# Performance work log

Measured on AMD Instinct MI355X. Metric: run time of the kernel, lower is better.

Reference implementation:

```python
import jax, jax.numpy as jnp
import numpy as np

B, S = 2, 2048
N_DIM, N_HEADS = 2048, 16
Q_RANK, KV_RANK = 1536, 512
ROPE, NOPE, VD = 64, 128, 128
QK_HEAD = NOPE + ROPE  # 192
EPS = 1e-6


def _rmsnorm(x, w, eps=EPS):
    xf = x.astype(jnp.float32)
    norm = xf * jax.lax.rsqrt(jnp.mean(xf * xf, axis=-1, keepdims=True) + eps)
    return norm.astype(x.dtype) * w


def setup_inputs() -> dict:
    key = jax.random.key(0)
    ks = jax.random.split(key, 7)
    std = 0.006
    x = jax.random.normal(ks[0], (B, S, N_DIM), dtype=jnp.float32)
    # rotary frequencies: complex cis encoded as (cos, sin) pairs, [S, ROPE//2, 2]
    inv_freq = 1.0 / (10000.0 ** (np.arange(0, ROPE, 2, dtype=np.float32) / ROPE))
    t = np.arange(S, dtype=np.float32)
    ang = np.outer(t, inv_freq)  # [S, ROPE//2]
    freqs_cis = jnp.asarray(np.stack([np.cos(ang), np.sin(ang)], axis=-1))
    return {
        "x": x,
        "freqs_cis": freqs_cis,
        "wq_a": jax.random.normal(ks[1], (Q_RANK, N_DIM)) * std,
        "q_norm_w": jnp.ones((Q_RANK,), jnp.float32),
        "wq_b": jax.random.normal(ks[2], (N_HEADS * QK_HEAD, Q_RANK)) * std,
        "wkv_a": jax.random.normal(ks[3], (KV_RANK + ROPE, N_DIM)) * std,
        "kv_norm_w": jnp.ones((KV_RANK,), jnp.float32),
        "wkv_b": jax.random.normal(ks[4], (N_HEADS * (NOPE + VD), KV_RANK)) * std,
        "wo": jax.random.normal(ks[5], (N_DIM, N_HEADS * VD)) * std,
    }


def _apply_rope(x_pe, freqs_cis):
    # x_pe: [B, S, H, ROPE] viewed as complex pairs; freqs_cis: [S, ROPE//2, 2]
    xr = x_pe[..., 0::2].astype(jnp.float32)
    xi = x_pe[..., 1::2].astype(jnp.float32)
    cos = freqs_cis[None, :, None, :, 0]
    sin = freqs_cis[None, :, None, :, 1]
    or_ = xr * cos - xi * sin
    oi_ = xr * sin + xi * cos
    out = jnp.stack([or_, oi_], axis=-1).reshape(*x_pe.shape)
    return out.astype(x_pe.dtype)


def reference(x, freqs_cis, wq_a, q_norm_w, wq_b, wkv_a, kv_norm_w, wkv_b, wo):
    bsz, seq = x.shape[0], x.shape[1]
    # query path: low-rank down-proj -> RMSNorm -> up-proj
    q = _rmsnorm(x @ wq_a.T, q_norm_w) @ wq_b.T
    q = q.reshape(bsz, seq, N_HEADS, QK_HEAD)
    q_nope, q_pe = q[..., :NOPE], q[..., NOPE:]
    # kv path: joint latent + rope carrier
    c = x @ wkv_a.T
    kv_lat, k_pe = c[..., :KV_RANK], c[..., KV_RANK:]
    kv = _rmsnorm(kv_lat, kv_norm_w) @ wkv_b.T
    kv = kv.reshape(bsz, seq, N_HEADS, NOPE + VD)
    k_nope, v = kv[..., :NOPE], kv[..., NOPE:]
    # rotary on rope sub-dims (k_pe shared across heads)
    q_pe = _apply_rope(q_pe, freqs_cis)
    k_pe = _apply_rope(k_pe[:, :, None, :], freqs_cis)  # [B,S,1,ROPE]
    qf = jnp.concatenate([q_nope, q_pe], axis=-1)                      # [B,S,H,192]
    kf = jnp.concatenate(
        [k_nope, jnp.broadcast_to(k_pe, (bsz, seq, N_HEADS, ROPE))], axis=-1
    )
    # causal SDPA, scale = 1/sqrt(qk_head_dim)
    scale = 1.0 / jnp.sqrt(jnp.float32(QK_HEAD))
    scores = jnp.einsum("bqhd,bkhd->bhqk", qf, kf) * scale
    causal = jnp.tril(jnp.ones((seq, seq), dtype=bool))
    scores = jnp.where(causal[None, None], scores, jnp.finfo(scores.dtype).min)
    attn = jax.nn.softmax(scores, axis=-1)
    out = jnp.einsum("bhqk,bkhd->bqhd", attn, v).reshape(bsz, seq, N_HEADS * VD)
    return out @ wo.T
```

## Files before the change

### kernel.cpp

```cpp
#include <hip/hip_runtime.h>
#include <hip/hip_bf16.h>
#include <math.h>
#include <stdint.h>

#define TOK 4096
#define SEQ 2048
#define NDIM 2048
#define NH 16
#define QR 1536
#define KVR 512
#define NOPE_D 128
#define QKH 192
#define QDIM 3072
#define KVDIM 4096
#define CW 640
#define ODIM 2048

typedef __attribute__((ext_vector_type(4))) float f32x4;
typedef __attribute__((ext_vector_type(8))) __bf16 bf16x8;
typedef __attribute__((ext_vector_type(8))) unsigned short u16x8;
typedef __attribute__((ext_vector_type(4))) unsigned short u16x4;

__device__ inline unsigned short f2bf(float f) {
  union { float f; uint32_t u; } v; v.f = f;
  uint32_t r = (v.u + 0x7FFFu + ((v.u >> 16) & 1u)) >> 16;
  return (unsigned short)r;
}
__device__ inline float bf2f(unsigned short s) {
  union { uint32_t u; float f; } v; v.u = ((uint32_t)s) << 16;
  return v.f;
}

__device__ inline void gload16(const void* g, void* l) {
  __builtin_amdgcn_global_load_lds(
      (const __attribute__((address_space(1))) unsigned int*)g,
      (__attribute__((address_space(3))) unsigned int*)l, 16, 0, 0);
}

__global__ __launch_bounds__(256) void cvt_kernel(const float* __restrict__ in,
                                                  unsigned short* __restrict__ out, long n) {
  long i = ((long)blockIdx.x * 256 + threadIdx.x) * 4;
  if (i >= n) return;
  f32x4 v = *(const f32x4*)(in + i);
  u16x4 o;
  #pragma unroll
  for (int j = 0; j < 4; j++) o[j] = f2bf(v[j]);
  *(u16x4*)(out + i) = o;
}

__global__ __launch_bounds__(256) void zero_kernel(unsigned short* __restrict__ out, long n) {
  long i = ((long)blockIdx.x * 256 + threadIdx.x) * 4;
  if (i >= n) return;
  u16x4 z = {0, 0, 0, 0};
  *(u16x4*)(out + i) = z;
}

__device__ inline void storev(unsigned short* p, float v) { *p = f2bf(v); }
__device__ inline void storev(float* p, float v) { *p = v; }

template <typename OutT>
__global__ __launch_bounds__(256) void gemm_bt(
    const unsigned short* __restrict__ A, int lda,
    const unsigned short* __restrict__ B, int ldb,
    OutT* __restrict__ C, int ldc, int K) {
  __shared__ unsigned short lA[128 * 32];
  __shared__ unsigned short lB[128 * 32];
  const int tid = threadIdx.x;
  const int lane = tid & 63, wave = tid >> 6;
  const int wr = wave >> 1, wc = wave & 1;
  const int l16 = lane & 15, lhi = lane >> 4;
  const long bm = (long)blockIdx.y * 128, bn = (long)blockIdx.x * 128;
  f32x4 acc[4][4];
  #pragma unroll
  for (int m = 0; m < 4; m++)
    #pragma unroll
    for (int n = 0; n < 4; n++) acc[m][n] = (f32x4){0.f, 0.f, 0.f, 0.f};
  const int srow = wave * 16 + (lane >> 2);
  const int scol = (lane & 3) * 8;
  const unsigned short* Ag0 = A + (bm + srow) * lda + scol;
  const unsigned short* Ag1 = A + (bm + 64 + srow) * lda + scol;
  const unsigned short* Bg0 = B + (bn + srow) * ldb + scol;
  const unsigned short* Bg1 = B + (bn + 64 + srow) * ldb + scol;
  unsigned short* lA0 = &lA[wave * 512];
  unsigned short* lA1 = &lA[2048 + wave * 512];
  unsigned short* lB0 = &lB[wave * 512];
  unsigned short* lB1 = &lB[2048 + wave * 512];
  for (int k0 = 0; k0 < K; k0 += 32) {
    __syncthreads();
    gload16(Ag0 + k0, lA0);
    gload16(Ag1 + k0, lA1);
    gload16(Bg0 + k0, lB0);
    gload16(Bg1 + k0, lB1);
    __syncthreads();
    bf16x8 af[4], bfv[4];
    #pragma unroll
    for (int m = 0; m < 4; m++)
      af[m] = *(const bf16x8*)&lA[(wr * 64 + m * 16 + l16) * 32 + lhi * 8];
    #pragma unroll
    for (int n = 0; n < 4; n++)
      bfv[n] = *(const bf16x8*)&lB[(wc * 64 + n * 16 + l16) * 32 + lhi * 8];
    #pragma unroll
    for (int m = 0; m < 4; m++)
      #pragma unroll
      for (int n = 0; n < 4; n++)
        acc[m][n] = __builtin_amdgcn_mfma_f32_16x16x32_bf16(af[m], bfv[n], acc[m][n], 0, 0, 0);
  }
  #pragma unroll
  for (int m = 0; m < 4; m++)
    #pragma unroll
    for (int n = 0; n < 4; n++) {
      long row = bm + wr * 64 + m * 16 + lhi * 4;
      long col = bn + wc * 64 + n * 16 + l16;
      #pragma unroll
      for (int i = 0; i < 4; i++) storev(&C[(row + i) * ldc + col], acc[m][n][i]);
    }
}

__global__ __launch_bounds__(256) void rmsnorm_kernel(unsigned short* __restrict__ buf,
                                                      const float* __restrict__ w,
                                                      int width, int lda) {
  const int tid = threadIdx.x;
  unsigned short* p = buf + (long)blockIdx.x * lda;
  float ss = 0.f;
  const int nc = width >> 2;
  for (int c = tid; c < nc; c += 256) {
    u16x4 v = *(const u16x4*)(p + c * 4);
    #pragma unroll
    for (int j = 0; j < 4; j++) { float f = bf2f(v[j]); ss += f * f; }
  }
  #pragma unroll
  for (int off = 32; off; off >>= 1) ss += __shfl_xor(ss, off);
  __shared__ float red[4];
  if ((tid & 63) == 0) red[tid >> 6] = ss;
  __syncthreads();
  float tot = red[0] + red[1] + red[2] + red[3];
  float rn = rsqrtf(tot / (float)width + 1e-6f);
  for (int c = tid; c < nc; c += 256) {
    u16x4 v = *(const u16x4*)(p + c * 4);
    u16x4 o;
    #pragma unroll
    for (int j = 0; j < 4; j++) o[j] = f2bf(bf2f(v[j]) * rn * w[c * 4 + j]);
    *(u16x4*)(p + c * 4) = o;
  }
}

__global__ __launch_bounds__(256) void rope_q_kernel(unsigned short* __restrict__ q,
                                                     const float* __restrict__ fr) {
  int idx = blockIdx.x * 256 + threadIdx.x;
  int pair = idx & 31, h = (idx >> 5) & 15, tok = idx >> 9;
  int s = tok & (SEQ - 1);
  unsigned short* p = q + (long)tok * QDIM + h * QKH + NOPE_D + pair * 2;
  float c = fr[(s * 32 + pair) * 2 + 0], sn = fr[(s * 32 + pair) * 2 + 1];
  float xr = bf2f(p[0]), xi = bf2f(p[1]);
  p[0] = f2bf(xr * c - xi * sn);
  p[1] = f2bf(xr * sn + xi * c);
}

__global__ __launch_bounds__(256) void rope_k_kernel(unsigned short* __restrict__ cb,
                                                     const float* __restrict__ fr) {
  int idx = blockIdx.x * 256 + threadIdx.x;
  int pair = idx & 31, tok = idx >> 5;
  int s = tok & (SEQ - 1);
  unsigned short* p = cb + (long)tok * CW + KVR + pair * 2;
  float c = fr[(s * 32 + pair) * 2 + 0], sn = fr[(s * 32 + pair) * 2 + 1];
  float xr = bf2f(p[0]), xi = bf2f(p[1]);
  p[0] = f2bf(xr * c - xi * sn);
  p[1] = f2bf(xr * sn + xi * c);
}

__global__ __launch_bounds__(512, 2) void attn_kernel(
    const unsigned short* __restrict__ qb,
    const unsigned short* __restrict__ kvb,
    const unsigned short* __restrict__ cb,
    unsigned short* __restrict__ ao) {
  const int bi = blockIdx.x;
  const int pr = bi & 7, h = (bi >> 3) & 15, b = bi >> 7;
  const int tid = threadIdx.x, wave = tid >> 6, lane = tid & 63;
  const int l16 = lane & 15, lhi = lane >> 4;
  const long tbase = (long)b * SEQ;
  __shared__ unsigned short lK[64][192];
  __shared__ unsigned short lV[128][64];
  __shared__ unsigned short lP[8][16][72];
  const float scale = 0.0721687836f;
  const int sw = l16 & 7;
  u16x8 kreg[3];
  u16x8 vreg[2];
  const int vpr = tid & 31, vd0 = (tid >> 5) * 8;

  auto load_tile = [&](int k0) {
    #pragma unroll
    for (int it = 0; it < 3; it++) {
      int c = tid + it * 512;
      int row = c / 24, ch = c % 24;
      const unsigned short* src = (ch < 16)
          ? kvb + (tbase + k0 + row) * KVDIM + h * 256 + ch * 8
          : cb + (tbase + k0 + row) * CW + KVR + (ch - 16) * 8;
      kreg[it] = *(const u16x8*)src;
    }
    const unsigned short* v0 = kvb + (tbase + k0 + 2 * vpr) * KVDIM + h * 256 + 128 + vd0;
    vreg[0] = *(const u16x8*)v0;
    vreg[1] = *(const u16x8*)(v0 + KVDIM);
  };
  auto write_tile = [&]() {
    #pragma unroll
    for (int it = 0; it < 3; it++) {
      int c = tid + it * 512;
      int row = c / 24, ch = c % 24;
      *(u16x8*)&lK[row][(ch ^ (row & 7)) * 8] = kreg[it];
    }
    #pragma unroll
    for (int j = 0; j < 8; j++)
      *(uint32_t*)&lV[vd0 + j][(2 * vpr) ^ (j << 3)] =
          (uint32_t)vreg[0][j] | ((uint32_t)vreg[1][j] << 16);
  };

  for (int sub = 0; sub < 2; sub++) {
    const int qt = sub ? (15 - pr) : pr;
    const int q0 = qt * 128;
    bf16x8 qf[6];
    {
      const unsigned short* qg = qb + (tbase + q0 + wave * 16 + l16) * QDIM + h * QKH;
      #pragma unroll
      for (int d = 0; d < 6; d++) qf[d] = *(const bf16x8*)(qg + d * 32 + lhi * 8);
    }
    f32x4 oacc[8];
    #pragma unroll
    for (int n = 0; n < 8; n++) oacc[n] = (f32x4){0.f, 0.f, 0.f, 0.f};
    float mr[4], lr[4];
    #pragma unroll
    for (int i = 0; i < 4; i++) { mr[i] = -1e30f; lr[i] = 0.f; }

    const int nkt = 2 * qt + 2;
    load_tile(0);
    for (int kt = 0; kt < nkt; kt++) {
      const int k0 = kt * 64;
      __syncthreads();
      write_tile();
      __syncthreads();
      if (kt + 1 < nkt) load_tile((kt + 1) * 64);
      f32x4 sc[4];
      #pragma unroll
      for (int ks = 0; ks < 4; ks++) {
        sc[ks] = (f32x4){0.f, 0.f, 0.f, 0.f};
        #pragma unroll
        for (int d = 0; d < 6; d++) {
          bf16x8 kf = *(const bf16x8*)&lK[ks * 16 + l16][((4 * d + lhi) ^ sw) * 8];
          sc[ks] = __builtin_amdgcn_mfma_f32_16x16x32_bf16(qf[d], kf, sc[ks], 0, 0, 0);
        }
      }
      #pragma unroll
      for (int ks = 0; ks < 4; ks++)
        #pragma unroll
        for (int i = 0; i < 4; i++) {
          float v = sc[ks][i] * scale;
          if ((k0 + ks * 16 + l16) > (q0 + wave * 16 + lhi * 4 + i)) v = -1e30f;
          sc[ks][i] = v;
        }
      float fac[4];
      #pragma unroll
      for (int i = 0; i < 4; i++) {
        float mx = fmaxf(fmaxf(sc[0][i], sc[1][i]), fmaxf(sc[2][i], sc[3][i]));
        #pragma unroll
        for (int off = 1; off < 16; off <<= 1) mx = fmaxf(mx, __shfl_xor(mx, off));
        float mn = fmaxf(mr[i], mx);
        fac[i] = exp2f((mr[i] - mn) * 1.44269504f);
        mr[i] = mn;
      }
      float rs[4] = {0.f, 0.f, 0.f, 0.f};
      #pragma unroll
      for (int ks = 0; ks < 4; ks++)
        #pragma unroll
        for (int i = 0; i < 4; i++) {
          float pv = exp2f((sc[ks][i] - mr[i]) * 1.44269504f);
          rs[i] += pv;
          lP[wave][lhi * 4 + i][ks * 16 + l16] = f2bf(pv);
        }
      #pragma unroll
      for (int i = 0; i < 4; i++) {
        float r = rs[i];
        #pragma unroll
        for (int off = 1; off < 16; off <<= 1) r += __shfl_xor(r, off);
        lr[i] = lr[i] * fac[i] + r;
      }
      #pragma unroll
      for (int n = 0; n < 8; n++) {
        f32x4 t = oacc[n];
        t[0] *= fac[0]; t[1] *= fac[1]; t[2] *= fac[2]; t[3] *= fac[3];
        oacc[n] = t;
      }
      #pragma unroll
      for (int kk = 0; kk < 2; kk++) {
        bf16x8 pf = *(const bf16x8*)&lP[wave][l16][kk * 32 + lhi * 8];
        #pragma unroll
        for (int n = 0; n < 8; n++) {
          bf16x8 vf = *(const bf16x8*)&lV[n * 16 + l16][((kk * 4 + lhi) ^ sw) * 8];
          oacc[n] = __builtin_amdgcn_mfma_f32_16x16x32_bf16(pf, vf, oacc[n], 0, 0, 0);
        }
      }
    }
    #pragma unroll
    for (int n = 0; n < 8; n++)
      #pragma unroll
      for (int i = 0; i < 4; i++) {
        long row = tbase + q0 + wave * 16 + lhi * 4 + i;
        ao[row * ODIM + h * 128 + n * 16 + l16] = f2bf(oacc[n][i] / lr[i]);
      }
  }
}

extern "C" void kernel_launch(void* const* d_in, const int* in_sizes, int n_in,
                              void* d_out, int out_size, void* d_ws, size_t ws_size,
                              hipStream_t stream) {
  const float* x = (const float*)d_in[0];
  const float* fr = (const float*)d_in[1];
  const float* wq_a = (const float*)d_in[2];
  const float* qnw = (const float*)d_in[3];
  const float* wq_b = (const float*)d_in[4];
  const float* wkv_a = (const float*)d_in[5];
  const float* kvnw = (const float*)d_in[6];
  const float* wkv_b = (const float*)d_in[7];
  const float* wo = (const float*)d_in[8];
  float* out = (float*)d_out;

  char* ws = (char*)d_ws;
  size_t o = 0;
  unsigned short* xb = (unsigned short*)(ws + o);    o += (size_t)TOK * NDIM * 2;
  unsigned short* wqab = (unsigned short*)(ws + o);  o += (size_t)QR * NDIM * 2;
  unsigned short* wqbb = (unsigned short*)(ws + o);  o += (size_t)QDIM * QR * 2;
  unsigned short* wkvab = (unsigned short*)(ws + o); o += (size_t)CW * NDIM * 2;
  unsigned short* wkvbb = (unsigned short*)(ws + o); o += (size_t)KVDIM * KVR * 2;
  unsigned short* wob = (unsigned short*)(ws + o);   o += (size_t)NDIM * ODIM * 2;
  unsigned short* cq = (unsigned short*)(ws + o);    o += (size_t)TOK * QR * 2;
  unsigned short* qbuf = (unsigned short*)(ws + o);  o += (size_t)TOK * QDIM * 2;
  unsigned short* cbuf = (unsigned short*)(ws + o);  o += (size_t)TOK * CW * 2;
  unsigned short* kvbuf = (unsigned short*)(ws + o); o += (size_t)TOK * KVDIM * 2;
  unsigned short* aout = (unsigned short*)(ws + o);  o += (size_t)TOK * ODIM * 2;

  cvt_kernel<<<(TOK * (long)NDIM) / 1024, 256, 0, stream>>>(x, xb, (long)TOK * NDIM);
  cvt_kernel<<<((long)QR * NDIM) / 1024, 256, 0, stream>>>(wq_a, wqab, (long)QR * NDIM);
  cvt_kernel<<<((long)QDIM * QR) / 1024, 256, 0, stream>>>(wq_b, wqbb, (long)QDIM * QR);
  cvt_kernel<<<((long)576 * NDIM) / 1024, 256, 0, stream>>>(wkv_a, wkvab, (long)576 * NDIM);
  zero_kernel<<<((long)64 * NDIM) / 1024, 256, 0, stream>>>(wkvab + (size_t)576 * NDIM,
                                                            (long)64 * NDIM);
  cvt_kernel<<<((long)KVDIM * KVR) / 1024, 256, 0, stream>>>(wkv_b, wkvbb, (long)KVDIM * KVR);
  cvt_kernel<<<((long)NDIM * ODIM) / 1024, 256, 0, stream>>>(wo, wob, (long)NDIM * ODIM);

  dim3 blk(256);
  gemm_bt<unsigned short><<<dim3(QR / 128, TOK / 128), blk, 0, stream>>>(
      xb, NDIM, wqab, NDIM, cq, QR, NDIM);
  gemm_bt<unsigned short><<<dim3(CW / 128, TOK / 128), blk, 0, stream>>>(
      xb, NDIM, wkvab, NDIM, cbuf, CW, NDIM);
  rmsnorm_kernel<<<TOK, 256, 0, stream>>>(cq, qnw, QR, QR);
  rmsnorm_kernel<<<TOK, 256, 0, stream>>>(cbuf, kvnw, KVR, CW);
  gemm_bt<unsigned short><<<dim3(QDIM / 128, TOK / 128), blk, 0, stream>>>(
      cq, QR, wqbb, QR, qbuf, QDIM, QR);
  gemm_bt<unsigned short><<<dim3(KVDIM / 128, TOK / 128), blk, 0, stream>>>(
      cbuf, CW, wkvbb, KVR, kvbuf, KVDIM, KVR);
  rope_q_kernel<<<(TOK * NH * 32) / 256, 256, 0, stream>>>(qbuf, fr);
  rope_k_kernel<<<(TOK * 32) / 256, 256, 0, stream>>>(cbuf, fr);
  attn_kernel<<<dim3(256, 1, 1), 512, 0, stream>>>(qbuf, kvbuf, cbuf, aout);
  gemm_bt<float><<<dim3(ODIM / 128, TOK / 128), blk, 0, stream>>>(
      aout, ODIM, wob, ODIM, out, ODIM, ODIM);
}
```

Measured before the change: 520.0 us.

## Double-buffer GEMM LDS, merge down-projections, skip mask off diagonal

```diff
diff --git a/kernel.cpp b/kernel.cpp
--- a/kernel.cpp
+++ b/kernel.cpp
@@ -13,7 +13,7 @@
 #define QKH 192
 #define QDIM 3072
 #define KVDIM 4096
-#define CW 640
+#define CSTR 2176
 #define ODIM 2048
 
 typedef __attribute__((ext_vector_type(4))) float f32x4;
@@ -63,8 +63,8 @@
     const unsigned short* __restrict__ A, int lda,
     const unsigned short* __restrict__ B, int ldb,
     OutT* __restrict__ C, int ldc, int K) {
-  __shared__ unsigned short lA[128 * 32];
-  __shared__ unsigned short lB[128 * 32];
+  __shared__ unsigned short lA[2][128 * 32];
+  __shared__ unsigned short lB[2][128 * 32];
   const int tid = threadIdx.x;
   const int lane = tid & 63, wave = tid >> 6;
   const int wr = wave >> 1, wc = wave & 1;
@@ -81,29 +81,38 @@
   const unsigned short* Ag1 = A + (bm + 64 + srow) * lda + scol;
   const unsigned short* Bg0 = B + (bn + srow) * ldb + scol;
   const unsigned short* Bg1 = B + (bn + 64 + srow) * ldb + scol;
-  unsigned short* lA0 = &lA[wave * 512];
-  unsigned short* lA1 = &lA[2048 + wave * 512];
-  unsigned short* lB0 = &lB[wave * 512];
-  unsigned short* lB1 = &lB[2048 + wave * 512];
-  for (int k0 = 0; k0 < K; k0 += 32) {
-    __syncthreads();
-    gload16(Ag0 + k0, lA0);
-    gload16(Ag1 + k0, lA1);
-    gload16(Bg0 + k0, lB0);
-    gload16(Bg1 + k0, lB1);
-    __syncthreads();
+  auto stage = [&](int buf, int k0) {
+    gload16(Ag0 + k0, &lA[buf][wave * 512]);
+    gload16(Ag1 + k0, &lA[buf][2048 + wave * 512]);
+    gload16(Bg0 + k0, &lB[buf][wave * 512]);
+    gload16(Bg1 + k0, &lB[buf][2048 + wave * 512]);
+  };
+  const int nt = K >> 5;
+  stage(0, 0);
+  for (int t = 0; t < nt; ++t) {
+    const int cur = t & 1;
+    if (t + 1 < nt) {
+      stage(cur ^ 1, (t + 1) * 32);
+      asm volatile("s_waitcnt vmcnt(4)" ::: "memory");
+    } else {
+      asm volatile("s_waitcnt vmcnt(0)" ::: "memory");
+    }
+    __builtin_amdgcn_s_barrier();
     bf16x8 af[4], bfv[4];
     #pragma unroll
     for (int m = 0; m < 4; m++)
-      af[m] = *(const bf16x8*)&lA[(wr * 64 + m * 16 + l16) * 32 + lhi * 8];
+      af[m] = *(const bf16x8*)&lA[cur][(wr * 64 + m * 16 + l16) * 32 + lhi * 8];
     #pragma unroll
     for (int n = 0; n < 4; n++)
-      bfv[n] = *(const bf16x8*)&lB[(wc * 64 + n * 16 + l16) * 32 + lhi * 8];
+      bfv[n] = *(const bf16x8*)&lB[cur][(wc * 64 + n * 16 + l16) * 32 + lhi * 8];
     #pragma unroll
     for (int m = 0; m < 4; m++)
       #pragma unroll
       for (int n = 0; n < 4; n++)
         acc[m][n] = __builtin_amdgcn_mfma_f32_16x16x32_bf16(af[m], bfv[n], acc[m][n], 0, 0, 0);
+    asm volatile("s_waitcnt lgkmcnt(0)" ::: "memory");
+    __builtin_amdgcn_sched_barrier(0);
+    __builtin_amdgcn_s_barrier();
   }
   #pragma unroll
   for (int m = 0; m < 4; m++)
@@ -161,7 +170,7 @@
   int idx = blockIdx.x * 256 + threadIdx.x;
   int pair = idx & 31, tok = idx >> 5;
   int s = tok & (SEQ - 1);
-  unsigned short* p = cb + (long)tok * CW + KVR + pair * 2;
+  unsigned short* p = cb + (long)tok * CSTR + KVR + pair * 2;
   float c = fr[(s * 32 + pair) * 2 + 0], sn = fr[(s * 32 + pair) * 2 + 1];
   float xr = bf2f(p[0]), xi = bf2f(p[1]);
   p[0] = f2bf(xr * c - xi * sn);
@@ -194,7 +203,7 @@
       int row = c / 24, ch = c % 24;
       const unsigned short* src = (ch < 16)
           ? kvb + (tbase + k0 + row) * KVDIM + h * 256 + ch * 8
-          : cb + (tbase + k0 + row) * CW + KVR + (ch - 16) * 8;
+          : cb + (tbase + k0 + row) * CSTR + KVR + (ch - 16) * 8;
       kreg[it] = *(const u16x8*)src;
     }
     const unsigned short* v0 = kvb + (tbase + k0 + 2 * vpr) * KVDIM + h * 256 + 128 + vd0;
@@ -229,6 +238,7 @@
     float mr[4], lr[4];
     #pragma unroll
     for (int i = 0; i < 4; i++) { mr[i] = -1e30f; lr[i] = 0.f; }
+    const int qrow = q0 + wave * 16 + lhi * 4;
 
     const int nkt = 2 * qt + 2;
     load_tile(0);
@@ -251,11 +261,16 @@
       #pragma unroll
       for (int ks = 0; ks < 4; ks++)
         #pragma unroll
-        for (int i = 0; i < 4; i++) {
-          float v = sc[ks][i] * scale;
-          if ((k0 + ks * 16 + l16) > (q0 + wave * 16 + lhi * 4 + i)) v = -1e30f;
-          sc[ks][i] = v;
+        for (int i = 0; i < 4; i++) sc[ks][i] *= scale;
+      if (kt >= 2 * qt) {
+        #pragma unroll
+        for (int ks = 0; ks < 4; ks++) {
+          const int kcol = k0 + ks * 16 + l16;
+          #pragma unroll
+          for (int i = 0; i < 4; i++)
+            if (kcol > qrow + i) sc[ks][i] = -1e30f;
         }
+      }
       float fac[4];
       #pragma unroll
       for (int i = 0; i < 4; i++) {
@@ -325,40 +340,38 @@
   char* ws = (char*)d_ws;
   size_t o = 0;
   unsigned short* xb = (unsigned short*)(ws + o);    o += (size_t)TOK * NDIM * 2;
-  unsigned short* wqab = (unsigned short*)(ws + o);  o += (size_t)QR * NDIM * 2;
+  unsigned short* wcomb = (unsigned short*)(ws + o); o += (size_t)CSTR * NDIM * 2;
   unsigned short* wqbb = (unsigned short*)(ws + o);  o += (size_t)QDIM * QR * 2;
-  unsigned short* wkvab = (unsigned short*)(ws + o); o += (size_t)CW * NDIM * 2;
   unsigned short* wkvbb = (unsigned short*)(ws + o); o += (size_t)KVDIM * KVR * 2;
   unsigned short* wob = (unsigned short*)(ws + o);   o += (size_t)NDIM * ODIM * 2;
-  unsigned short* cq = (unsigned short*)(ws + o);    o += (size_t)TOK * QR * 2;
+  unsigned short* cw = (unsigned short*)(ws + o);    o += (size_t)TOK * CSTR * 2;
   unsigned short* qbuf = (unsigned short*)(ws + o);  o += (size_t)TOK * QDIM * 2;
-  unsigned short* cbuf = (unsigned short*)(ws + o);  o += (size_t)TOK * CW * 2;
   unsigned short* kvbuf = (unsigned short*)(ws + o); o += (size_t)TOK * KVDIM * 2;
   unsigned short* aout = (unsigned short*)(ws + o);  o += (size_t)TOK * ODIM * 2;
+  unsigned short* ckv = cw + QR;
 
   cvt_kernel<<<(TOK * (long)NDIM) / 1024, 256, 0, stream>>>(x, xb, (long)TOK * NDIM);
-  cvt_kernel<<<((long)QR * NDIM) / 1024, 256, 0, stream>>>(wq_a, wqab, (long)QR * NDIM);
+  cvt_kernel<<<((long)QR * NDIM) / 1024, 256, 0, stream>>>(wq_a, wcomb, (long)QR * NDIM);
+  cvt_kernel<<<((long)576 * NDIM) / 1024, 256, 0, stream>>>(
+      wkv_a, wcomb + (size_t)QR * NDIM, (long)576 * NDIM);
+  zero_kernel<<<((long)64 * NDIM) / 1024, 256, 0, stream>>>(
+      wcomb + (size_t)(QR + 576) * NDIM, (long)64 * NDIM);
   cvt_kernel<<<((long)QDIM * QR) / 1024, 256, 0, stream>>>(wq_b, wqbb, (long)QDIM * QR);
-  cvt_kernel<<<((long)576 * NDIM) / 1024, 256, 0, stream>>>(wkv_a, wkvab, (long)576 * NDIM);
-  zero_kernel<<<((long)64 * NDIM) / 1024, 256, 0, stream>>>(wkvab + (size_t)576 * NDIM,
-                                                            (long)64 * NDIM);
   cvt_kernel<<<((long)KVDIM * KVR) / 1024, 256, 0, stream>>>(wkv_b, wkvbb, (long)KVDIM * KVR);
   cvt_kernel<<<((long)NDIM * ODIM) / 1024, 256, 0, stream>>>(wo, wob, (long)NDIM * ODIM);
 
   dim3 blk(256);
-  gemm_bt<unsigned short><<<dim3(QR / 128, TOK / 128), blk, 0, stream>>>(
-      xb, NDIM, wqab, NDIM, cq, QR, NDIM);
-  gemm_bt<unsigned short><<<dim3(CW / 128, TOK / 128), blk, 0, stream>>>(
-      xb, NDIM, wkvab, NDIM, cbuf, CW, NDIM);
-  rmsnorm_kernel<<<TOK, 256, 0, stream>>>(cq, qnw, QR, QR);
-  rmsnorm_kernel<<<TOK, 256, 0, stream>>>(cbuf, kvnw, KVR, CW);
+  gemm_bt<unsigned short><<<dim3(CSTR / 128, TOK / 128), blk, 0, stream>>>(
+      xb, NDIM, wcomb, NDIM, cw, CSTR, NDIM);
+  rmsnorm_kernel<<<TOK, 256, 0, stream>>>(cw, qnw, QR, CSTR);
+  rmsnorm_kernel<<<TOK, 256, 0, stream>>>(ckv, kvnw, KVR, CSTR);
   gemm_bt<unsigned short><<<dim3(QDIM / 128, TOK / 128), blk, 0, stream>>>(
-      cq, QR, wqbb, QR, qbuf, QDIM, QR);
+      cw, CSTR, wqbb, QR, qbuf, QDIM, QR);
   gemm_bt<unsigned short><<<dim3(KVDIM / 128, TOK / 128), blk, 0, stream>>>(
-      cbuf, CW, wkvbb, KVR, kvbuf, KVDIM, KVR);
+      ckv, CSTR, wkvbb, KVR, kvbuf, KVDIM, KVR);
   rope_q_kernel<<<(TOK * NH * 32) / 256, 256, 0, stream>>>(qbuf, fr);
-  rope_k_kernel<<<(TOK * 32) / 256, 256, 0, stream>>>(cbuf, fr);
-  attn_kernel<<<dim3(256, 1, 1), 512, 0, stream>>>(qbuf, kvbuf, cbuf, aout);
+  rope_k_kernel<<<(TOK * 32) / 256, 256, 0, stream>>>(ckv, fr);
+  attn_kernel<<<dim3(256, 1, 1), 512, 0, stream>>>(qbuf, kvbuf, ckv, aout);
   gemm_bt<float><<<dim3(ODIM / 128, TOK / 128), blk, 0, stream>>>(
       aout, ODIM, wob, ODIM, out, ODIM, ODIM);
 }
```

Measured after the change: 463.5 us. 1.12x faster.
